# Performance work log

Hardware: AMD Instinct MI355X
Metric: run time of the kernel (lower is better)

## Reference

```python
import jax, jax.numpy as jnp
import numpy as np

B, S, D, H = 2, 2048, 768, 12
DK = D // H

def setup_inputs() -> dict:
    key = jax.random.key(0)
    ks = jax.random.split(key, 11)
    sc = 0.02
    inp = {
        'Q': jax.random.normal(ks[0], (B, S, D), jnp.float32),
        'K': jax.random.normal(ks[1], (B, S, D), jnp.float32),
        'V': jax.random.normal(ks[2], (B, S, D), jnp.float32),
        # causal mask, broadcastable over batch and heads (1 = keep, 0 = mask)
        'mask': jnp.tril(jnp.ones((S, S), jnp.int32))[None, None, :, :],
        'Wq': jax.random.normal(ks[3], (D, D), jnp.float32) * sc,
        'bq': jax.random.normal(ks[4], (D,), jnp.float32) * sc,
        'Wk': jax.random.normal(ks[5], (D, D), jnp.float32) * sc,
        'bk': jax.random.normal(ks[6], (D,), jnp.float32) * sc,
        'Wv': jax.random.normal(ks[7], (D, D), jnp.float32) * sc,
        'bv': jax.random.normal(ks[8], (D,), jnp.float32) * sc,
        'Wo': jax.random.normal(ks[9], (D, D), jnp.float32) * sc,
        'bo': jax.random.normal(ks[10], (D,), jnp.float32) * sc,
    }
    return inp

def _split_heads(x):
    # [B,S,D] -> [B,H,S,DK]
    return x.reshape(B, S, H, DK).transpose(0, 2, 1, 3)

def reference(Q, K, V, mask, Wq, bq, Wk, bk, Wv, bv, Wo, bo):
    # torch Linear: y = x @ W.T + b
    q = _split_heads(Q @ Wq.T + bq)
    k = _split_heads(K @ Wk.T + bk)
    v = _split_heads(V @ Wv.T + bv)
    scores = jnp.einsum('bhqd,bhkd->bhqk', q, k) / jnp.sqrt(jnp.float32(DK))
    scores = jnp.where(mask == 0, jnp.float32(-1e9), scores)
    attn = jax.nn.softmax(scores, axis=-1)
    out = jnp.einsum('bhqk,bhkd->bhqd', attn, v)  # [B,H,S,DK]
    out = out.transpose(0, 2, 1, 3).reshape(B, S, D)
    return out @ Wo.T + bo
```

## Files before the change

kernel.cpp:

```cpp
#include <hip/hip_runtime.h>
#include <hip/hip_bf16.h>

#define H_  12
#define S_  2048
#define D_  768
#define DK_ 64

typedef __bf16 bf16x8 __attribute__((ext_vector_type(8)));
typedef __bf16 bf16x4 __attribute__((ext_vector_type(4)));
typedef float  f32x4  __attribute__((ext_vector_type(4)));

#define QSCALE 0.1803368801111137f

__device__ inline float exp2_fast(float x) {
  return __builtin_amdgcn_exp2f(x);
}

__device__ inline f32x4 mfma_bf16(bf16x8 a, bf16x8 b, f32x4 c) {
  return __builtin_amdgcn_mfma_f32_16x16x32_bf16(a, b, c, 0, 0, 0);
}

__device__ inline void gload16(const void* g, void* l) {
  __builtin_amdgcn_global_load_lds(
      (const __attribute__((address_space(1))) void*)g,
      (__attribute__((address_space(3))) void*)l, 16, 0, 0);
}

__device__ inline bf16x8 cvt2bf16(f32x4 a, f32x4 b) {
  bf16x8 r;
  r[0] = (__bf16)a[0]; r[1] = (__bf16)a[1];
  r[2] = (__bf16)a[2]; r[3] = (__bf16)a[3];
  r[4] = (__bf16)b[0]; r[5] = (__bf16)b[1];
  r[6] = (__bf16)b[2]; r[7] = (__bf16)b[3];
  return r;
}

__global__ __launch_bounds__(256)
void conv_w(const float* __restrict__ Wq, const float* __restrict__ Wk,
            const float* __restrict__ Wv, const float* __restrict__ Wo,
            __hip_bfloat16* __restrict__ out)
{
  const int i8 = blockIdx.x * 256 + threadIdx.x;
  const int mat = i8 / 73728;
  const int off = (i8 - mat * 73728) * 8;
  const float* src = (mat == 0) ? Wq : (mat == 1) ? Wk : (mat == 2) ? Wv : Wo;
  f32x4 a = *(const f32x4*)(src + off);
  f32x4 b = *(const f32x4*)(src + off + 4);
  *(bf16x8*)(out + (size_t)mat * 589824 + off) = cvt2bf16(a, b);
}

__global__ __launch_bounds__(256, 3)
void qkv_proj(const float* __restrict__ Q, const float* __restrict__ K,
              const float* __restrict__ V,
              const __hip_bfloat16* __restrict__ Wb,
              const float* __restrict__ bq, const float* __restrict__ bk,
              const float* __restrict__ bv,
              __hip_bfloat16* __restrict__ q_ws,
              __hip_bfloat16* __restrict__ k_ws,
              __hip_bfloat16* __restrict__ vT_ws)
{
  __shared__ alignas(16) __hip_bfloat16 Ald[128 * 32];
  __shared__ alignas(16) __hip_bfloat16 Bld[128 * 32];

  const int z = blockIdx.z;
  const float* X    = (z == 0) ? Q  : (z == 1) ? K  : V;
  const float* bias = (z == 0) ? bq : (z == 1) ? bk : bv;
  const __hip_bfloat16* Wz = Wb + (size_t)z * 589824;
  __hip_bfloat16* out = (z == 0) ? q_ws : (z == 1) ? k_ws : vT_ws;
  const bool vmode = (z == 2);
  const float osc = (z == 0) ? QSCALE : 1.0f;

  const int t    = threadIdx.x;
  const int w    = t >> 6;
  const int lane = t & 63;
  const int l15  = lane & 15;
  const int quad = lane >> 4;
  const int m0 = blockIdx.x * 128;
  const int n0 = blockIdx.y * 128;
  const int wm = (w >> 1) * 64;
  const int wn = (w & 1) * 64;

  __hip_bfloat16* Xbuf = vmode ? Bld : Ald;
  __hip_bfloat16* Wbuf = vmode ? Ald : Bld;

  const f32x4 fzero = {0.f, 0.f, 0.f, 0.f};
  f32x4 acc[4][4];
#pragma unroll
  for (int i = 0; i < 4; ++i)
#pragma unroll
    for (int j = 0; j < 4; ++j) acc[i][j] = fzero;

  const int ar = t >> 2, ac = t & 3;
  const int sw = ac ^ ((ar >> 1) & 3);
  const float* As0 = X + (size_t)(m0 + ar) * D_ + ac * 8;
  const float* As1 = X + (size_t)(m0 + ar + 64) * D_ + ac * 8;
  __hip_bfloat16* Xw0 = &Xbuf[((ar)      * 4 + sw) * 8];
  __hip_bfloat16* Xw1 = &Xbuf[((ar + 64) * 4 + sw) * 8];

  const int bp = (t & 3) ^ (((t >> 2) >> 1) & 3);
  const __hip_bfloat16* Bs0 = Wz + (size_t)(n0 + (t >> 2)) * D_ + bp * 8;
  const __hip_bfloat16* Bs1 = Wz + (size_t)(n0 + (t >> 2) + 64) * D_ + bp * 8;
  __hip_bfloat16* Wd0 = &Wbuf[t * 8];
  __hip_bfloat16* Wd1 = &Wbuf[(t + 256) * 8];

  int agrn[4], bgrn[4];
#pragma unroll
  for (int i = 0; i < 4; ++i) {
    int row = wm + 16 * i + l15;
    agrn[i] = (row * 4 + (quad ^ ((row >> 1) & 3))) * 8;
    row = wn + 16 * i + l15;
    bgrn[i] = (row * 4 + (quad ^ ((row >> 1) & 3))) * 8;
  }

  f32x4 a00 = *(const f32x4*)As0, a01 = *(const f32x4*)(As0 + 4);
  f32x4 a10 = *(const f32x4*)As1, a11 = *(const f32x4*)(As1 + 4);

  for (int k0 = 0; k0 < D_; k0 += 32) {
    *(bf16x8*)Xw0 = cvt2bf16(a00, a01);
    *(bf16x8*)Xw1 = cvt2bf16(a10, a11);
    gload16(Bs0 + k0, Wd0);
    gload16(Bs1 + k0, Wd1);
    __syncthreads();

    const int kn = k0 + 32;
    if (kn < D_) {
      a00 = *(const f32x4*)(As0 + kn); a01 = *(const f32x4*)(As0 + kn + 4);
      a10 = *(const f32x4*)(As1 + kn); a11 = *(const f32x4*)(As1 + kn + 4);
    }

    bf16x8 af[4], bfr[4];
#pragma unroll
    for (int i = 0; i < 4; ++i) af[i]  = *(const bf16x8*)&Ald[agrn[i]];
#pragma unroll
    for (int j = 0; j < 4; ++j) bfr[j] = *(const bf16x8*)&Bld[bgrn[j]];
#pragma unroll
    for (int i = 0; i < 4; ++i)
#pragma unroll
      for (int j = 0; j < 4; ++j)
        acc[i][j] = mfma_bf16(af[i], bfr[j], acc[i][j]);
    __syncthreads();
  }

  if (!vmode) {
#pragma unroll
    for (int j = 0; j < 4; ++j) {
      const int n_g = n0 + wn + 16 * j + l15;
      const float bv = bias[n_g];
      const int hh = n_g >> 6, dk = n_g & (DK_ - 1);
#pragma unroll
      for (int i = 0; i < 4; ++i) {
        const int mbase = m0 + wm + 16 * i + quad * 4;
#pragma unroll
        for (int r = 0; r < 4; ++r) {
          const int m_g = mbase + r;
          const int bb = m_g >> 11, ss = m_g & (S_ - 1);
          const float vout = (acc[i][j][r] + bv) * osc;
          out[(((size_t)(bb * H_ + hh)) * S_ + ss) * DK_ + dk] =
              __float2bfloat16(vout);
        }
      }
    }
  } else {
#pragma unroll
    for (int i = 0; i < 4; ++i) {
      const int nbase = n0 + wm + 16 * i + quad * 4;
#pragma unroll
      for (int r = 0; r < 4; ++r) {
        const int n_g = nbase + r;
        const float bv = bias[n_g];
        const int hh = n_g >> 6, dk = n_g & (DK_ - 1);
#pragma unroll
        for (int j = 0; j < 4; ++j) {
          const int m_g = m0 + wn + 16 * j + l15;
          const int bb = m_g >> 11, ss = m_g & (S_ - 1);
          const int ssp = (ss & ~31) | (((ss >> 2) & 3) << 3) |
                          (((ss >> 4) & 1) << 2) | (ss & 3);
          out[(((size_t)(bb * H_ + hh)) * DK_ + dk) * S_ + ssp] =
              __float2bfloat16(acc[i][j][r] + bv);
        }
      }
    }
  }
}

__global__ __launch_bounds__(256, 4)
void o_proj(const __hip_bfloat16* __restrict__ Xb,
            const __hip_bfloat16* __restrict__ Wob,
            const float* __restrict__ bias,
            float* __restrict__ outf)
{
  __shared__ alignas(16) __hip_bfloat16 Ald[64 * 32];
  __shared__ alignas(16) __hip_bfloat16 Bld[128 * 32];

  const int t    = threadIdx.x;
  const int w    = t >> 6;
  const int lane = t & 63;
  const int l15  = lane & 15;
  const int quad = lane >> 4;
  const int m0 = blockIdx.x * 64;
  const int n0 = blockIdx.y * 128;
  const int wm = (w >> 1) * 32;
  const int wn = (w & 1) * 64;

  const f32x4 fzero = {0.f, 0.f, 0.f, 0.f};
  f32x4 acc[2][4];
#pragma unroll
  for (int i = 0; i < 2; ++i)
#pragma unroll
    for (int j = 0; j < 4; ++j) acc[i][j] = fzero;

  const int ap = (t & 3) ^ (((t >> 2) >> 1) & 3);
  const __hip_bfloat16* As  = Xb  + (size_t)(m0 + (t >> 2)) * D_ + ap * 8;
  const __hip_bfloat16* Bs0 = Wob + (size_t)(n0 + (t >> 2)) * D_ + ap * 8;
  const __hip_bfloat16* Bs1 = Wob + (size_t)(n0 + (t >> 2) + 64) * D_ + ap * 8;
  __hip_bfloat16* Ad  = &Ald[t * 8];
  __hip_bfloat16* Bd0 = &Bld[t * 8];
  __hip_bfloat16* Bd1 = &Bld[(t + 256) * 8];

  int agrn[2], bgrn[4];
#pragma unroll
  for (int i = 0; i < 2; ++i) {
    const int row = wm + 16 * i + l15;
    agrn[i] = (row * 4 + (quad ^ ((row >> 1) & 3))) * 8;
  }
#pragma unroll
  for (int j = 0; j < 4; ++j) {
    const int row = wn + 16 * j + l15;
    bgrn[j] = (row * 4 + (quad ^ ((row >> 1) & 3))) * 8;
  }

  for (int k0 = 0; k0 < D_; k0 += 32) {
    gload16(As + k0, Ad);
    gload16(Bs0 + k0, Bd0);
    gload16(Bs1 + k0, Bd1);
    __syncthreads();

    bf16x8 af[2], bfr[4];
#pragma unroll
    for (int i = 0; i < 2; ++i) af[i]  = *(const bf16x8*)&Ald[agrn[i]];
#pragma unroll
    for (int j = 0; j < 4; ++j) bfr[j] = *(const bf16x8*)&Bld[bgrn[j]];
#pragma unroll
    for (int i = 0; i < 2; ++i)
#pragma unroll
      for (int j = 0; j < 4; ++j)
        acc[i][j] = mfma_bf16(af[i], bfr[j], acc[i][j]);
    __syncthreads();
  }

#pragma unroll
  for (int j = 0; j < 4; ++j) {
    const int n_g = n0 + wn + 16 * j + l15;
    const float bv = bias[n_g];
#pragma unroll
    for (int i = 0; i < 2; ++i) {
      const int mbase = m0 + wm + 16 * i + quad * 4;
#pragma unroll
      for (int r = 0; r < 4; ++r)
        outf[(size_t)(mbase + r) * D_ + n_g] = acc[i][j][r] + bv;
    }
  }
}

__global__ __launch_bounds__(256, 4)
void flash_attn(const __hip_bfloat16* __restrict__ q_ws,
                const __hip_bfloat16* __restrict__ k_ws,
                const __hip_bfloat16* __restrict__ vT_ws,
                __hip_bfloat16* __restrict__ o_ws)
{
  __shared__ alignas(16) __hip_bfloat16 Kld[128][72];
  __shared__ alignas(16) __hip_bfloat16 Vld[64][136];

  const int t = threadIdx.x, w = t >> 6, lane = t & 63;
  const int l15 = lane & 15, quad = lane >> 4;

  const int id   = blockIdx.x;
  const int slot = id & 7;
  const int jj   = id >> 3;
  const int grp  = jj >> 5;
  const int bh   = slot + 8 * grp;
  const int x    = ((jj & 31) + 13 * grp) & 31;

  const int b = bh / H_, h = bh % H_;
  const int tLo = x, tHi = 63 - x;
  const int flip = x & 1;
  const int myTile = ((w >> 1) ^ flip) ? tHi : tLo;
  const int qbase = myTile * 32 + 16 * (w & 1);
  const int qg = qbase + l15;
  const int myNkt = (myTile >> 2) + 1;
  const int nktT  = (tHi >> 2) + 1;
  const size_t hbase = (size_t)bh * S_ * DK_;
  const size_t vtb   = (size_t)bh * DK_ * S_;

  bf16x8 qf[2];
#pragma unroll
  for (int kk = 0; kk < 2; ++kk)
    qf[kk] = *(const bf16x8*)(q_ws + hbase + (size_t)qg * DK_ + kk * 32 + quad * 8);

  const f32x4 fzero = {0.f, 0.f, 0.f, 0.f};
  const f32x4 cinit = {-16.f, -16.f, -16.f, -16.f};
  bf16x8 ones;
#pragma unroll
  for (int i = 0; i < 8; ++i) ones[i] = (__bf16)1.0f;

  f32x4 accO[4];
#pragma unroll
  for (int jd = 0; jd < 4; ++jd) accO[jd] = fzero;
  f32x4 accL = fzero;

  const int tr = t >> 3, kg = t & 7;
  const int tv = t >> 4, vg = t & 15;
  const __hip_bfloat16* Kbase = k_ws + hbase + (size_t)tr * DK_ + kg * 8;
  const __hip_bfloat16* Vbase = vT_ws + vtb + (size_t)tv * S_ + vg * 8;

  bf16x8 rK[4], rV[4];
#pragma unroll
  for (int it = 0; it < 4; ++it) {
    rK[it] = *(const bf16x8*)(Kbase + (size_t)(32 * it) * DK_);
    rV[it] = *(const bf16x8*)(Vbase + (size_t)(16 * it) * S_);
  }

  for (int kt = 0; kt < nktT; ++kt) {
#pragma unroll
    for (int it = 0; it < 4; ++it) {
      *(bf16x8*)&Kld[32 * it + tr][kg * 8] = rK[it];
      *(bf16x8*)&Vld[16 * it + tv][vg * 8] = rV[it];
    }
    __syncthreads();

    if (kt + 1 < nktT) {
      const int k0n = (kt + 1) * 128;
#pragma unroll
      for (int it = 0; it < 4; ++it) {
        rK[it] = *(const bf16x8*)(Kbase + (size_t)(k0n + 32 * it) * DK_);
        rV[it] = *(const bf16x8*)(Vbase + (size_t)(16 * it) * S_ + k0n);
      }
    }

    if (kt < myNkt) {
      const int k0 = kt * 128;
      f32x4 st[8];
      __builtin_amdgcn_s_setprio(1);
#pragma unroll
      for (int j = 0; j < 8; ++j) {
        bf16x8 kf0 = *(const bf16x8*)&Kld[16 * j + l15][quad * 8];
        bf16x8 kf1 = *(const bf16x8*)&Kld[16 * j + l15][32 + quad * 8];
        st[j] = mfma_bf16(kf0, qf[0], cinit);
        st[j] = mfma_bf16(kf1, qf[1], st[j]);
      }
      __builtin_amdgcn_s_setprio(0);

      if (kt == myNkt - 1) {
#pragma unroll
        for (int j = 0; j < 8; ++j)
#pragma unroll
          for (int r = 0; r < 4; ++r) {
            const int kcg = k0 + 16 * j + quad * 4 + r;
            if (kcg > qg) st[j][r] = -1.0e9f;
          }
      }

      bf16x8 pB[4];
#pragma unroll
      for (int s = 0; s < 4; ++s)
#pragma unroll
        for (int i = 0; i < 4; ++i) {
          pB[s][i]     = (__bf16)exp2_fast(st[2 * s][i]);
          pB[s][4 + i] = (__bf16)exp2_fast(st[2 * s + 1][i]);
        }

      __builtin_amdgcn_s_setprio(1);
#pragma unroll
      for (int s = 0; s < 4; ++s) {
#pragma unroll
        for (int jd = 0; jd < 4; ++jd) {
          bf16x8 vf = *(const bf16x8*)&Vld[16 * jd + l15][32 * s + quad * 8];
          accO[jd] = mfma_bf16(vf, pB[s], accO[jd]);
        }
        accL = mfma_bf16(ones, pB[s], accL);
      }
      __builtin_amdgcn_s_setprio(0);
    }
    __syncthreads();
  }

  const float inv = 1.f / accL[0];
#pragma unroll
  for (int jd = 0; jd < 4; ++jd) {
    bf16x4 ov;
#pragma unroll
    for (int r = 0; r < 4; ++r) ov[r] = (__bf16)(accO[jd][r] * inv);
    *(bf16x4*)(o_ws + ((size_t)b * S_ + qg) * D_ + h * DK_ + 16 * jd + quad * 4) = ov;
  }
}

extern "C" void kernel_launch(void* const* d_in, const int* in_sizes, int n_in,
                              void* d_out, int out_size, void* d_ws, size_t ws_size,
                              hipStream_t stream) {
  (void)in_sizes; (void)n_in; (void)out_size; (void)ws_size;
  const float* Q  = (const float*)d_in[0];
  const float* K  = (const float*)d_in[1];
  const float* V  = (const float*)d_in[2];
  const float* Wq = (const float*)d_in[4];
  const float* bq = (const float*)d_in[5];
  const float* Wk = (const float*)d_in[6];
  const float* bk = (const float*)d_in[7];
  const float* Wv = (const float*)d_in[8];
  const float* bv = (const float*)d_in[9];
  const float* Wo = (const float*)d_in[10];
  const float* bo = (const float*)d_in[11];
  float* out = (float*)d_out;

  const size_t WEL = (size_t)4 * 589824;
  const size_t NEL = (size_t)2 * S_ * D_;
  __hip_bfloat16* wb    = (__hip_bfloat16*)d_ws;
  __hip_bfloat16* q_ws  = wb + WEL;
  __hip_bfloat16* k_ws  = q_ws  + NEL;
  __hip_bfloat16* vT_ws = k_ws  + NEL;
  __hip_bfloat16* o_ws  = vT_ws + NEL;

  conv_w<<<1152, 256, 0, stream>>>(Wq, Wk, Wv, Wo, wb);
  qkv_proj<<<dim3(32, 6, 3), 256, 0, stream>>>(Q, K, V, wb, bq, bk, bv,
                                               q_ws, k_ws, vT_ws);
  flash_attn<<<768, 256, 0, stream>>>(q_ws, k_ws, vT_ws, o_ws);
  o_proj<<<dim3(64, 6), 256, 0, stream>>>(o_ws, wb + (size_t)3 * 589824, bo, out);
}
```

Measured before the change: 183.1 us.

## Pre-convert Q/K/V activations to bf16 and load both GEMM operands via LDS DMA

The fp32 Q/K/V activations are now converted to bf16 in the same pre-pass kernel that converts the weights, writing them to a new workspace region. The QKV projection then streams both operands straight into LDS with global_load_lds instead of doing register fp32 loads, conversion and ds_write for the activation tile. MFMA blocks are wrapped in s_setprio. This removes per-iteration conversion work and register staging in the GEMM. The cost is an extra full write and read of the converted activations through global memory, plus a larger conversion launch.

```diff
diff --git a/kernel.cpp b/kernel.cpp
--- a/kernel.cpp
+++ b/kernel.cpp
@@ -11,6 +11,9 @@
 typedef float  f32x4  __attribute__((ext_vector_type(4)));
 
 #define QSCALE 0.1803368801111137f
+
+#define WEL 589824
+#define XEL 3145728
 
 __device__ inline float exp2_fast(float x) {
   return __builtin_amdgcn_exp2f(x);
@@ -36,22 +39,36 @@
 }
 
 __global__ __launch_bounds__(256)
-void conv_w(const float* __restrict__ Wq, const float* __restrict__ Wk,
-            const float* __restrict__ Wv, const float* __restrict__ Wo,
-            __hip_bfloat16* __restrict__ out)
+void conv_in(const float* __restrict__ Wq, const float* __restrict__ Wk,
+             const float* __restrict__ Wv, const float* __restrict__ Wo,
+             const float* __restrict__ Q, const float* __restrict__ K,
+             const float* __restrict__ V,
+             __hip_bfloat16* __restrict__ wout,
+             __hip_bfloat16* __restrict__ xout)
 {
   const int i8 = blockIdx.x * 256 + threadIdx.x;
-  const int mat = i8 / 73728;
-  const int off = (i8 - mat * 73728) * 8;
-  const float* src = (mat == 0) ? Wq : (mat == 1) ? Wk : (mat == 2) ? Wv : Wo;
+  const float* src;
+  __hip_bfloat16* dst;
+  int off;
+  if (i8 < 294912) {
+    const int mat = i8 / 73728;
+    off = (i8 - mat * 73728) * 8;
+    src = (mat == 0) ? Wq : (mat == 1) ? Wk : (mat == 2) ? Wv : Wo;
+    dst = wout + (size_t)mat * WEL;
+  } else {
+    const int j = i8 - 294912;
+    const int mat = j / 393216;
+    off = (j - mat * 393216) * 8;
+    src = (mat == 0) ? Q : (mat == 1) ? K : V;
+    dst = xout + (size_t)mat * XEL;
+  }
   f32x4 a = *(const f32x4*)(src + off);
   f32x4 b = *(const f32x4*)(src + off + 4);
-  *(bf16x8*)(out + (size_t)mat * 589824 + off) = cvt2bf16(a, b);
+  *(bf16x8*)(dst + off) = cvt2bf16(a, b);
 }
 
 __global__ __launch_bounds__(256, 3)
-void qkv_proj(const float* __restrict__ Q, const float* __restrict__ K,
-              const float* __restrict__ V,
+void qkv_proj(const __hip_bfloat16* __restrict__ Xall,
               const __hip_bfloat16* __restrict__ Wb,
               const float* __restrict__ bq, const float* __restrict__ bk,
               const float* __restrict__ bv,
@@ -63,9 +80,9 @@
   __shared__ alignas(16) __hip_bfloat16 Bld[128 * 32];
 
   const int z = blockIdx.z;
-  const float* X    = (z == 0) ? Q  : (z == 1) ? K  : V;
+  const __hip_bfloat16* Xb = Xall + (size_t)z * XEL;
+  const __hip_bfloat16* Wz = Wb + (size_t)z * WEL;
   const float* bias = (z == 0) ? bq : (z == 1) ? bk : bv;
-  const __hip_bfloat16* Wz = Wb + (size_t)z * 589824;
   __hip_bfloat16* out = (z == 0) ? q_ws : (z == 1) ? k_ws : vT_ws;
   const bool vmode = (z == 2);
   const float osc = (z == 0) ? QSCALE : 1.0f;
@@ -80,9 +97,6 @@
   const int wm = (w >> 1) * 64;
   const int wn = (w & 1) * 64;
 
-  __hip_bfloat16* Xbuf = vmode ? Bld : Ald;
-  __hip_bfloat16* Wbuf = vmode ? Ald : Bld;
-
   const f32x4 fzero = {0.f, 0.f, 0.f, 0.f};
   f32x4 acc[4][4];
 #pragma unroll
@@ -90,18 +104,19 @@
 #pragma unroll
     for (int j = 0; j < 4; ++j) acc[i][j] = fzero;
 
-  const int ar = t >> 2, ac = t & 3;
-  const int sw = ac ^ ((ar >> 1) & 3);
-  const float* As0 = X + (size_t)(m0 + ar) * D_ + ac * 8;
-  const float* As1 = X + (size_t)(m0 + ar + 64) * D_ + ac * 8;
-  __hip_bfloat16* Xw0 = &Xbuf[((ar)      * 4 + sw) * 8];
-  __hip_bfloat16* Xw1 = &Xbuf[((ar + 64) * 4 + sw) * 8];
-
   const int bp = (t & 3) ^ (((t >> 2) >> 1) & 3);
-  const __hip_bfloat16* Bs0 = Wz + (size_t)(n0 + (t >> 2)) * D_ + bp * 8;
-  const __hip_bfloat16* Bs1 = Wz + (size_t)(n0 + (t >> 2) + 64) * D_ + bp * 8;
-  __hip_bfloat16* Wd0 = &Wbuf[t * 8];
-  __hip_bfloat16* Wd1 = &Wbuf[(t + 256) * 8];
+  const __hip_bfloat16* Arow = vmode ? (Wz + (size_t)n0 * D_)
+                                     : (Xb + (size_t)m0 * D_);
+  const __hip_bfloat16* Brow = vmode ? (Xb + (size_t)m0 * D_)
+                                     : (Wz + (size_t)n0 * D_);
+  const __hip_bfloat16* SA0 = Arow + (size_t)(t >> 2) * D_ + bp * 8;
+  const __hip_bfloat16* SA1 = Arow + (size_t)((t >> 2) + 64) * D_ + bp * 8;
+  const __hip_bfloat16* SB0 = Brow + (size_t)(t >> 2) * D_ + bp * 8;
+  const __hip_bfloat16* SB1 = Brow + (size_t)((t >> 2) + 64) * D_ + bp * 8;
+  __hip_bfloat16* Ad0 = &Ald[t * 8];
+  __hip_bfloat16* Ad1 = &Ald[(t + 256) * 8];
+  __hip_bfloat16* Bd0 = &Bld[t * 8];
+  __hip_bfloat16* Bd1 = &Bld[(t + 256) * 8];
 
   int agrn[4], bgrn[4];
 #pragma unroll
@@ -112,32 +127,25 @@
     bgrn[i] = (row * 4 + (quad ^ ((row >> 1) & 3))) * 8;
   }
 
-  f32x4 a00 = *(const f32x4*)As0, a01 = *(const f32x4*)(As0 + 4);
-  f32x4 a10 = *(const f32x4*)As1, a11 = *(const f32x4*)(As1 + 4);
-
   for (int k0 = 0; k0 < D_; k0 += 32) {
-    *(bf16x8*)Xw0 = cvt2bf16(a00, a01);
-    *(bf16x8*)Xw1 = cvt2bf16(a10, a11);
-    gload16(Bs0 + k0, Wd0);
-    gload16(Bs1 + k0, Wd1);
-    __syncthreads();
-
-    const int kn = k0 + 32;
-    if (kn < D_) {
-      a00 = *(const f32x4*)(As0 + kn); a01 = *(const f32x4*)(As0 + kn + 4);
-      a10 = *(const f32x4*)(As1 + kn); a11 = *(const f32x4*)(As1 + kn + 4);
-    }
+    gload16(SA0 + k0, Ad0);
+    gload16(SA1 + k0, Ad1);
+    gload16(SB0 + k0, Bd0);
+    gload16(SB1 + k0, Bd1);
+    __syncthreads();
 
     bf16x8 af[4], bfr[4];
 #pragma unroll
     for (int i = 0; i < 4; ++i) af[i]  = *(const bf16x8*)&Ald[agrn[i]];
 #pragma unroll
     for (int j = 0; j < 4; ++j) bfr[j] = *(const bf16x8*)&Bld[bgrn[j]];
+    __builtin_amdgcn_s_setprio(1);
 #pragma unroll
     for (int i = 0; i < 4; ++i)
 #pragma unroll
       for (int j = 0; j < 4; ++j)
         acc[i][j] = mfma_bf16(af[i], bfr[j], acc[i][j]);
+    __builtin_amdgcn_s_setprio(0);
     __syncthreads();
   }
 
@@ -411,17 +419,17 @@
   const float* bo = (const float*)d_in[11];
   float* out = (float*)d_out;
 
-  const size_t WEL = (size_t)4 * 589824;
   const size_t NEL = (size_t)2 * S_ * D_;
   __hip_bfloat16* wb    = (__hip_bfloat16*)d_ws;
-  __hip_bfloat16* q_ws  = wb + WEL;
+  __hip_bfloat16* q_ws  = wb + (size_t)4 * WEL;
   __hip_bfloat16* k_ws  = q_ws  + NEL;
   __hip_bfloat16* vT_ws = k_ws  + NEL;
   __hip_bfloat16* o_ws  = vT_ws + NEL;
-
-  conv_w<<<1152, 256, 0, stream>>>(Wq, Wk, Wv, Wo, wb);
-  qkv_proj<<<dim3(32, 6, 3), 256, 0, stream>>>(Q, K, V, wb, bq, bk, bv,
+  __hip_bfloat16* xb    = o_ws  + NEL;
+
+  conv_in<<<5760, 256, 0, stream>>>(Wq, Wk, Wv, Wo, Q, K, V, wb, xb);
+  qkv_proj<<<dim3(32, 6, 3), 256, 0, stream>>>(xb, wb, bq, bk, bv,
                                                q_ws, k_ws, vT_ws);
   flash_attn<<<768, 256, 0, stream>>>(q_ws, k_ws, vT_ws, o_ws);
-  o_proj<<<dim3(64, 6), 256, 0, stream>>>(o_ws, wb + (size_t)3 * 589824, bo, out);
-}
+  o_proj<<<dim3(64, 6), 256, 0, stream>>>(o_ws, wb + (size_t)3 * WEL, bo, out);
+}
```

After: 182.4 us. Within noise of the previous version (-0.4%).

## Load V fragments directly from global memory instead of staging through LDS

Applied to the files above, without the earlier changes.

Removes the shared-memory V tile and its cooperative register-prefetch/store. Each wave now reads its V^T MFMA operands straight from global memory (L2/cache), double-buffered in registers across the four PV sub-steps. This cuts LDS traffic, LDS footprint and store work per iteration. The cost is that the four waves of a block each fetch the same V data redundantly, and global-load latency now sits closer to the MFMAs with less prefetch distance.

```diff
diff --git a/kernel.cpp b/kernel.cpp
--- a/kernel.cpp
+++ b/kernel.cpp
@@ -269,7 +269,6 @@
                 __hip_bfloat16* __restrict__ o_ws)
 {
   __shared__ alignas(16) __hip_bfloat16 Kld[128][72];
-  __shared__ alignas(16) __hip_bfloat16 Vld[64][136];
 
   const int t = threadIdx.x, w = t >> 6, lane = t & 63;
   const int l15 = lane & 15, quad = lane >> 4;
@@ -309,36 +308,38 @@
   f32x4 accL = fzero;
 
   const int tr = t >> 3, kg = t & 7;
-  const int tv = t >> 4, vg = t & 15;
   const __hip_bfloat16* Kbase = k_ws + hbase + (size_t)tr * DK_ + kg * 8;
-  const __hip_bfloat16* Vbase = vT_ws + vtb + (size_t)tv * S_ + vg * 8;
-
-  bf16x8 rK[4], rV[4];
-#pragma unroll
-  for (int it = 0; it < 4; ++it) {
+  const __hip_bfloat16* VL = vT_ws + vtb + (size_t)l15 * S_ + quad * 8;
+
+  bf16x8 rK[4];
+#pragma unroll
+  for (int it = 0; it < 4; ++it)
     rK[it] = *(const bf16x8*)(Kbase + (size_t)(32 * it) * DK_);
-    rV[it] = *(const bf16x8*)(Vbase + (size_t)(16 * it) * S_);
-  }
 
   for (int kt = 0; kt < nktT; ++kt) {
 #pragma unroll
-    for (int it = 0; it < 4; ++it) {
+    for (int it = 0; it < 4; ++it)
       *(bf16x8*)&Kld[32 * it + tr][kg * 8] = rK[it];
-      *(bf16x8*)&Vld[16 * it + tv][vg * 8] = rV[it];
-    }
     __syncthreads();
 
     if (kt + 1 < nktT) {
       const int k0n = (kt + 1) * 128;
 #pragma unroll
-      for (int it = 0; it < 4; ++it) {
+      for (int it = 0; it < 4; ++it)
         rK[it] = *(const bf16x8*)(Kbase + (size_t)(k0n + 32 * it) * DK_);
-        rV[it] = *(const bf16x8*)(Vbase + (size_t)(16 * it) * S_ + k0n);
-      }
     }
 
     if (kt < myNkt) {
       const int k0 = kt * 128;
+      const __hip_bfloat16* Vk = VL + k0;
+
+      bf16x8 vfA[4], vfB[4];
+#pragma unroll
+      for (int jd = 0; jd < 4; ++jd) {
+        vfA[jd] = *(const bf16x8*)(Vk + (size_t)jd * 16 * S_);
+        vfB[jd] = *(const bf16x8*)(Vk + (size_t)jd * 16 * S_ + 32);
+      }
+
       f32x4 st[8];
       __builtin_amdgcn_s_setprio(1);
 #pragma unroll
@@ -371,14 +372,27 @@
 
       __builtin_amdgcn_s_setprio(1);
 #pragma unroll
-      for (int s = 0; s < 4; ++s) {
-#pragma unroll
-        for (int jd = 0; jd < 4; ++jd) {
-          bf16x8 vf = *(const bf16x8*)&Vld[16 * jd + l15][32 * s + quad * 8];
-          accO[jd] = mfma_bf16(vf, pB[s], accO[jd]);
-        }
-        accL = mfma_bf16(ones, pB[s], accL);
-      }
+      for (int jd = 0; jd < 4; ++jd)
+        accO[jd] = mfma_bf16(vfA[jd], pB[0], accO[jd]);
+      accL = mfma_bf16(ones, pB[0], accL);
+#pragma unroll
+      for (int jd = 0; jd < 4; ++jd)
+        vfA[jd] = *(const bf16x8*)(Vk + (size_t)jd * 16 * S_ + 64);
+#pragma unroll
+      for (int jd = 0; jd < 4; ++jd)
+        accO[jd] = mfma_bf16(vfB[jd], pB[1], accO[jd]);
+      accL = mfma_bf16(ones, pB[1], accL);
+#pragma unroll
+      for (int jd = 0; jd < 4; ++jd)
+        vfB[jd] = *(const bf16x8*)(Vk + (size_t)jd * 16 * S_ + 96);
+#pragma unroll
+      for (int jd = 0; jd < 4; ++jd)
+        accO[jd] = mfma_bf16(vfA[jd], pB[2], accO[jd]);
+      accL = mfma_bf16(ones, pB[2], accL);
+#pragma unroll
+      for (int jd = 0; jd < 4; ++jd)
+        accO[jd] = mfma_bf16(vfB[jd], pB[3], accO[jd]);
+      accL = mfma_bf16(ones, pB[3], accL);
       __builtin_amdgcn_s_setprio(0);
     }
     __syncthreads();
```

Result: slower. 208.5 us (+13.8%).

## Give each attention wave two query sub-tiles to reuse K/V fragments

Applied to the files above, without the earlier changes.

The flash attention kernel drops from 4 waves to 2 per block. Each wave now handles 32 query rows (two 16-row sub-tiles) instead of 16, so every K and V fragment read from LDS feeds two MFMAs. Each thread now loads 8 K/V chunks per tile instead of 4. This halves LDS fragment reads per MFMA, at the cost of roughly double the accumulator and prefetch registers and fewer waves per block, with launch bounds changed to (128,2).

```diff
diff --git a/kernel.cpp b/kernel.cpp
--- a/kernel.cpp
+++ b/kernel.cpp
@@ -262,7 +262,7 @@
   }
 }
 
-__global__ __launch_bounds__(256, 4)
+__global__ __launch_bounds__(128, 2)
 void flash_attn(const __hip_bfloat16* __restrict__ q_ws,
                 const __hip_bfloat16* __restrict__ k_ws,
                 const __hip_bfloat16* __restrict__ vT_ws,
@@ -284,18 +284,20 @@
   const int b = bh / H_, h = bh % H_;
   const int tLo = x, tHi = 63 - x;
   const int flip = x & 1;
-  const int myTile = ((w >> 1) ^ flip) ? tHi : tLo;
-  const int qbase = myTile * 32 + 16 * (w & 1);
-  const int qg = qbase + l15;
+  const int myTile = (w ^ flip) ? tHi : tLo;
+  const int qg0 = myTile * 32 + l15;
+  const int qg1 = qg0 + 16;
   const int myNkt = (myTile >> 2) + 1;
   const int nktT  = (tHi >> 2) + 1;
   const size_t hbase = (size_t)bh * S_ * DK_;
   const size_t vtb   = (size_t)bh * DK_ * S_;
 
-  bf16x8 qf[2];
-#pragma unroll
-  for (int kk = 0; kk < 2; ++kk)
-    qf[kk] = *(const bf16x8*)(q_ws + hbase + (size_t)qg * DK_ + kk * 32 + quad * 8);
+  bf16x8 qf0[2], qf1[2];
+#pragma unroll
+  for (int kk = 0; kk < 2; ++kk) {
+    qf0[kk] = *(const bf16x8*)(q_ws + hbase + (size_t)qg0 * DK_ + kk * 32 + quad * 8);
+    qf1[kk] = *(const bf16x8*)(q_ws + hbase + (size_t)qg1 * DK_ + kk * 32 + quad * 8);
+  }
 
   const f32x4 fzero = {0.f, 0.f, 0.f, 0.f};
   const f32x4 cinit = {-16.f, -16.f, -16.f, -16.f};
@@ -303,94 +305,109 @@
 #pragma unroll
   for (int i = 0; i < 8; ++i) ones[i] = (__bf16)1.0f;
 
-  f32x4 accO[4];
-#pragma unroll
-  for (int jd = 0; jd < 4; ++jd) accO[jd] = fzero;
-  f32x4 accL = fzero;
-
-  const int tr = t >> 3, kg = t & 7;
-  const int tv = t >> 4, vg = t & 15;
-  const __hip_bfloat16* Kbase = k_ws + hbase + (size_t)tr * DK_ + kg * 8;
-  const __hip_bfloat16* Vbase = vT_ws + vtb + (size_t)tv * S_ + vg * 8;
-
-  bf16x8 rK[4], rV[4];
-#pragma unroll
-  for (int it = 0; it < 4; ++it) {
-    rK[it] = *(const bf16x8*)(Kbase + (size_t)(32 * it) * DK_);
-    rV[it] = *(const bf16x8*)(Vbase + (size_t)(16 * it) * S_);
+  f32x4 accO0[4], accO1[4];
+#pragma unroll
+  for (int jd = 0; jd < 4; ++jd) { accO0[jd] = fzero; accO1[jd] = fzero; }
+  f32x4 accL0 = fzero, accL1 = fzero;
+
+  const int kr = t >> 3, kc = t & 7;
+  const int vr = t >> 4, vc = t & 15;
+  const __hip_bfloat16* Kbase = k_ws + hbase + (size_t)kr * DK_ + kc * 8;
+  const __hip_bfloat16* Vbase = vT_ws + vtb + (size_t)vr * S_ + vc * 8;
+
+  bf16x8 rK[8], rV[8];
+#pragma unroll
+  for (int it = 0; it < 8; ++it) {
+    rK[it] = *(const bf16x8*)(Kbase + (size_t)(16 * it) * DK_);
+    rV[it] = *(const bf16x8*)(Vbase + (size_t)(8 * it) * S_);
   }
 
   for (int kt = 0; kt < nktT; ++kt) {
 #pragma unroll
-    for (int it = 0; it < 4; ++it) {
-      *(bf16x8*)&Kld[32 * it + tr][kg * 8] = rK[it];
-      *(bf16x8*)&Vld[16 * it + tv][vg * 8] = rV[it];
+    for (int it = 0; it < 8; ++it) {
+      *(bf16x8*)&Kld[16 * it + kr][kc * 8] = rK[it];
+      *(bf16x8*)&Vld[8 * it + vr][vc * 8] = rV[it];
     }
     __syncthreads();
 
     if (kt + 1 < nktT) {
       const int k0n = (kt + 1) * 128;
 #pragma unroll
-      for (int it = 0; it < 4; ++it) {
-        rK[it] = *(const bf16x8*)(Kbase + (size_t)(k0n + 32 * it) * DK_);
-        rV[it] = *(const bf16x8*)(Vbase + (size_t)(16 * it) * S_ + k0n);
+      for (int it = 0; it < 8; ++it) {
+        rK[it] = *(const bf16x8*)(Kbase + (size_t)(k0n + 16 * it) * DK_);
+        rV[it] = *(const bf16x8*)(Vbase + (size_t)(8 * it) * S_ + k0n);
       }
     }
 
     if (kt < myNkt) {
       const int k0 = kt * 128;
-      f32x4 st[8];
+      const bool maskt = (kt == myNkt - 1);
+
+      bf16x8 pB0[4], pB1[4];
       __builtin_amdgcn_s_setprio(1);
 #pragma unroll
-      for (int j = 0; j < 8; ++j) {
-        bf16x8 kf0 = *(const bf16x8*)&Kld[16 * j + l15][quad * 8];
-        bf16x8 kf1 = *(const bf16x8*)&Kld[16 * j + l15][32 + quad * 8];
-        st[j] = mfma_bf16(kf0, qf[0], cinit);
-        st[j] = mfma_bf16(kf1, qf[1], st[j]);
+      for (int s = 0; s < 4; ++s) {
+        bf16x8 kfa0 = *(const bf16x8*)&Kld[32 * s + l15][quad * 8];
+        bf16x8 kfa1 = *(const bf16x8*)&Kld[32 * s + l15][32 + quad * 8];
+        bf16x8 kfb0 = *(const bf16x8*)&Kld[32 * s + 16 + l15][quad * 8];
+        bf16x8 kfb1 = *(const bf16x8*)&Kld[32 * s + 16 + l15][32 + quad * 8];
+        f32x4 sa0 = mfma_bf16(kfa0, qf0[0], cinit);
+        sa0 = mfma_bf16(kfa1, qf0[1], sa0);
+        f32x4 sb0 = mfma_bf16(kfb0, qf0[0], cinit);
+        sb0 = mfma_bf16(kfb1, qf0[1], sb0);
+        f32x4 sa1 = mfma_bf16(kfa0, qf1[0], cinit);
+        sa1 = mfma_bf16(kfa1, qf1[1], sa1);
+        f32x4 sb1 = mfma_bf16(kfb0, qf1[0], cinit);
+        sb1 = mfma_bf16(kfb1, qf1[1], sb1);
+
+        if (maskt) {
+#pragma unroll
+          for (int r = 0; r < 4; ++r) {
+            const int ka = k0 + 32 * s + quad * 4 + r;
+            const int kb = ka + 16;
+            if (ka > qg0) sa0[r] = -1.0e9f;
+            if (kb > qg0) sb0[r] = -1.0e9f;
+            if (ka > qg1) sa1[r] = -1.0e9f;
+            if (kb > qg1) sb1[r] = -1.0e9f;
+          }
+        }
+#pragma unroll
+        for (int i = 0; i < 4; ++i) {
+          pB0[s][i]     = (__bf16)exp2_fast(sa0[i]);
+          pB0[s][4 + i] = (__bf16)exp2_fast(sb0[i]);
+          pB1[s][i]     = (__bf16)exp2_fast(sa1[i]);
+          pB1[s][4 + i] = (__bf16)exp2_fast(sb1[i]);
+        }
+      }
+
+#pragma unroll
+      for (int s = 0; s < 4; ++s) {
+#pragma unroll
+        for (int jd = 0; jd < 4; ++jd) {
+          bf16x8 vf = *(const bf16x8*)&Vld[16 * jd + l15][32 * s + quad * 8];
+          accO0[jd] = mfma_bf16(vf, pB0[s], accO0[jd]);
+          accO1[jd] = mfma_bf16(vf, pB1[s], accO1[jd]);
+        }
+        accL0 = mfma_bf16(ones, pB0[s], accL0);
+        accL1 = mfma_bf16(ones, pB1[s], accL1);
       }
       __builtin_amdgcn_s_setprio(0);
-
-      if (kt == myNkt - 1) {
-#pragma unroll
-        for (int j = 0; j < 8; ++j)
-#pragma unroll
-          for (int r = 0; r < 4; ++r) {
-            const int kcg = k0 + 16 * j + quad * 4 + r;
-            if (kcg > qg) st[j][r] = -1.0e9f;
-          }
-      }
-
-      bf16x8 pB[4];
-#pragma unroll
-      for (int s = 0; s < 4; ++s)
-#pragma unroll
-        for (int i = 0; i < 4; ++i) {
-          pB[s][i]     = (__bf16)exp2_fast(st[2 * s][i]);
-          pB[s][4 + i] = (__bf16)exp2_fast(st[2 * s + 1][i]);
-        }
-
-      __builtin_amdgcn_s_setprio(1);
-#pragma unroll
-      for (int s = 0; s < 4; ++s) {
-#pragma unroll
-        for (int jd = 0; jd < 4; ++jd) {
-          bf16x8 vf = *(const bf16x8*)&Vld[16 * jd + l15][32 * s + quad * 8];
-          accO[jd] = mfma_bf16(vf, pB[s], accO[jd]);
-        }
-        accL = mfma_bf16(ones, pB[s], accL);
-      }
-      __builtin_amdgcn_s_setprio(0);
-    }
-    __syncthreads();
-  }
-
-  const float inv = 1.f / accL[0];
+    }
+    __syncthreads();
+  }
+
+  const float inv0 = 1.f / accL0[0];
+  const float inv1 = 1.f / accL1[0];
 #pragma unroll
   for (int jd = 0; jd < 4; ++jd) {
-    bf16x4 ov;
-#pragma unroll
-    for (int r = 0; r < 4; ++r) ov[r] = (__bf16)(accO[jd][r] * inv);
-    *(bf16x4*)(o_ws + ((size_t)b * S_ + qg) * D_ + h * DK_ + 16 * jd + quad * 4) = ov;
+    bf16x4 ov0, ov1;
+#pragma unroll
+    for (int r = 0; r < 4; ++r) {
+      ov0[r] = (__bf16)(accO0[jd][r] * inv0);
+      ov1[r] = (__bf16)(accO1[jd][r] * inv1);
+    }
+    *(bf16x4*)(o_ws + ((size_t)b * S_ + qg0) * D_ + h * DK_ + 16 * jd + quad * 4) = ov0;
+    *(bf16x4*)(o_ws + ((size_t)b * S_ + qg1) * D_ + h * DK_ + 16 * jd + quad * 4) = ov1;
   }
 }
 
@@ -422,6 +439,6 @@
   conv_w<<<1152, 256, 0, stream>>>(Wq, Wk, Wv, Wo, wb);
   qkv_proj<<<dim3(32, 6, 3), 256, 0, stream>>>(Q, K, V, wb, bq, bk, bv,
                                                q_ws, k_ws, vT_ws);
-  flash_attn<<<768, 256, 0, stream>>>(q_ws, k_ws, vT_ws, o_ws);
+  flash_attn<<<768, 128, 0, stream>>>(q_ws, k_ws, vT_ws, o_ws);
   o_proj<<<dim3(64, 6), 256, 0, stream>>>(o_ws, wb + (size_t)3 * 589824, bo, out);
 }
```

Result: slower. 188.9 us (+3.1%).
